# Kernel tuning notes

Hardware: AMD Instinct MI355X
Metric: run time of the kernel (lower is better)

Reference implementation:

```python
import jax, jax.numpy as jnp
import numpy as np

M, K, N = 32, 4096, 12288


def setup_inputs() -> dict:
    key = jax.random.key(0)
    k1, k2, k3, k4 = jax.random.split(key, 4)
    x = jax.random.normal(k1, (M, K), dtype=jnp.float32)
    # uint8-valued packed weight (stored as int32 for harness compatibility, values in [0,256))
    weight_u8 = jax.random.randint(k2, (K, N), 0, 256, dtype=jnp.int32)
    # per-output-channel fp16 scale and zero-point
    scale = (jax.random.uniform(k3, (N,), dtype=jnp.float32) * 0.01 + 1e-3).astype(jnp.float16)
    zero = (jax.random.uniform(k4, (N,), dtype=jnp.float32) * 255.0).astype(jnp.float16)
    return {"x": x, "weight_u8": weight_u8, "scale": scale, "zero": zero}


def reference(x, weight_u8, scale, zero):
    # QuantMatmulCustom: dequantize uint8 weight with per-channel fp16 scale/zero, then matmul.
    # w_deq[k, n] = (w_u8[k, n] - zero[n]) * scale[n]
    w_deq = (weight_u8.astype(jnp.float32) - zero.astype(jnp.float32)[None, :]) * scale.astype(jnp.float32)[None, :]
    # [M, K] @ [K, N] -> [M, N]
    return jnp.einsum('mk,kn->mn', x, w_deq)
```

## Files before the change

kernel.cpp:

```cpp
#include <hip/hip_runtime.h>

#define M_DIM 32
#define K_DIM 4096
#define N_DIM 12288
#define SPLITK 8
#define KPER  (K_DIM / SPLITK)
#define NT    (KPER / 32)
#define BLK   512
#define NPB   128

using bf16x8 = __attribute__((ext_vector_type(8))) short;
using f32x4  = __attribute__((ext_vector_type(4))) float;

__global__ __launch_bounds__(256) void qmm_zero(float* __restrict__ out) {
    int i = blockIdx.x * 256 + threadIdx.x;
    ((float4*)out)[i] = make_float4(0.f, 0.f, 0.f, 0.f);
}

__device__ __forceinline__ void load_b(const int* __restrict__ wp, int t, int (&wv)[8]) {
    #pragma unroll
    for (int j = 0; j < 8; ++j)
        wv[j] = wp[(size_t)(t * 32 + j) * N_DIM];
}

__device__ __forceinline__ bf16x8 pack_b(const int (&wv)[8]) {
    bf16x8 b;
    #pragma unroll
    for (int j = 0; j < 8; ++j) {
        float f = (float)wv[j];
        b[j] = (short)(__float_as_uint(f) >> 16);
    }
    return b;
}

__global__ __launch_bounds__(BLK, 6) void qmm_main(const float* __restrict__ x,
                                                   const int* __restrict__ w,
                                                   float* __restrict__ out) {
    __shared__ short lds_a[NT * 2 * 64 * 8];

    const int tid  = threadIdx.x;
    const int lane = tid & 63;
    const int g    = lane >> 4;
    const int c    = lane & 15;
    const int wid  = tid >> 6;
    const int k0   = blockIdx.y * KPER;
    const int n0   = blockIdx.x * NPB + wid * 16;

    for (int s = tid; s < NT * 2 * 64; s += BLK) {
        const int l  = s & 63;
        const int h  = (s >> 6) & 1;
        const int kt = s >> 7;
        const int m  = 16 * h + (l & 15);
        const float* xp = x + (size_t)m * K_DIM + k0 + kt * 32 + 8 * (l >> 4);
        bf16x8 v;
        #pragma unroll
        for (int j = 0; j < 8; ++j) {
            unsigned u = __float_as_uint(xp[j]);
            u += 0x7FFFu + ((u >> 16) & 1u);
            v[j] = (short)(u >> 16);
        }
        *(bf16x8*)&lds_a[s * 8] = v;
    }
    __syncthreads();

    f32x4 acc0 = {0.f, 0.f, 0.f, 0.f};
    f32x4 acc1 = {0.f, 0.f, 0.f, 0.f};

    const int*   wp = w + (size_t)(k0 + 8 * g) * N_DIM + n0 + c;
    const short* la = lds_a + lane * 8;

    int wvA[8], wvB[8];
    load_b(wp, 0, wvA);
    #pragma unroll
    for (int t = 0; t < NT; t += 2) {
        if (t + 1 < NT) load_b(wp, t + 1, wvB);
        {
            bf16x8 bf = pack_b(wvA);
            bf16x8 a0 = *(const bf16x8*)&la[(size_t)(t * 2 + 0) * 512];
            bf16x8 a1 = *(const bf16x8*)&la[(size_t)(t * 2 + 1) * 512];
            acc0 = __builtin_amdgcn_mfma_f32_16x16x32_bf16(a0, bf, acc0, 0, 0, 0);
            acc1 = __builtin_amdgcn_mfma_f32_16x16x32_bf16(a1, bf, acc1, 0, 0, 0);
        }
        if (t + 2 < NT) load_b(wp, t + 2, wvA);
        if (t + 1 < NT) {
            bf16x8 bf = pack_b(wvB);
            bf16x8 a0 = *(const bf16x8*)&la[(size_t)((t + 1) * 2 + 0) * 512];
            bf16x8 a1 = *(const bf16x8*)&la[(size_t)((t + 1) * 2 + 1) * 512];
            acc0 = __builtin_amdgcn_mfma_f32_16x16x32_bf16(a0, bf, acc0, 0, 0, 0);
            acc1 = __builtin_amdgcn_mfma_f32_16x16x32_bf16(a1, bf, acc1, 0, 0, 0);
        }
    }

    #pragma unroll
    for (int i = 0; i < 4; ++i) {
        const int r = 4 * (lane >> 4) + i;
        atomicAdd(&out[(size_t)r * N_DIM + n0 + c], acc0[i]);
        atomicAdd(&out[(size_t)(16 + r) * N_DIM + n0 + c], acc1[i]);
    }
}

__global__ __launch_bounds__(256) void qmm_scale(const float* __restrict__ x,
                                                 const float* __restrict__ scale,
                                                 const float* __restrict__ zero,
                                                 float* __restrict__ out) {
    const int m = blockIdx.y;
    __shared__ float red[256];
    float s = 0.f;
    for (int k = threadIdx.x; k < K_DIM; k += 256)
        s += x[(size_t)m * K_DIM + k];
    red[threadIdx.x] = s;
    __syncthreads();
    #pragma unroll
    for (int off = 128; off > 0; off >>= 1) {
        if (threadIdx.x < off) red[threadIdx.x] += red[threadIdx.x + off];
        __syncthreads();
    }
    const float rowsum = red[0];

    const int n = blockIdx.x * 256 + threadIdx.x;
    const float v = out[(size_t)m * N_DIM + n];
    out[(size_t)m * N_DIM + n] = scale[n] * (v - zero[n] * rowsum);
}

extern "C" void kernel_launch(void* const* d_in, const int* in_sizes, int n_in,
                              void* d_out, int out_size, void* d_ws, size_t ws_size,
                              hipStream_t stream) {
    const float* x     = (const float*)d_in[0];
    const int*   w     = (const int*)d_in[1];
    const float* scale = (const float*)d_in[2];
    const float* zero  = (const float*)d_in[3];
    float* out = (float*)d_out;

    qmm_zero <<<dim3((M_DIM * N_DIM / 4) / 256), dim3(256), 0, stream>>>(out);
    qmm_main <<<dim3(N_DIM / NPB, SPLITK),       dim3(BLK), 0, stream>>>(x, w, out);
    qmm_scale<<<dim3(N_DIM / 256, M_DIM),        dim3(256), 0, stream>>>(x, scale, zero, out);
}
```

Before: 53.21 us.

## Double split-K, deepen weight prefetch, and reduce partials via workspace

Split-K goes from 8 to 16, and launch bounds drop from 6 to 4 waves. The weight-load pipeline becomes a three-deep register ring, with the first loads issued before the LDS barrier so they overlap the activation staging. When the workspace is large enough, each split writes its partial tile to a workspace slice instead of atomically adding, and a finalize kernel sums the slices and applies the zero-point and scale corrections. This drops the zero-fill kernel and the atomics but adds 16×M×N of float partial traffic to write and read back, and the deeper prefetch needs more registers.

```diff
diff --git a/kernel.cpp b/kernel.cpp
--- a/kernel.cpp
+++ b/kernel.cpp
@@ -3,7 +3,7 @@
 #define M_DIM 32
 #define K_DIM 4096
 #define N_DIM 12288
-#define SPLITK 8
+#define SPLITK 16
 #define KPER  (K_DIM / SPLITK)
 #define NT    (KPER / 32)
 #define BLK   512
@@ -11,11 +11,6 @@
 
 using bf16x8 = __attribute__((ext_vector_type(8))) short;
 using f32x4  = __attribute__((ext_vector_type(4))) float;
-
-__global__ __launch_bounds__(256) void qmm_zero(float* __restrict__ out) {
-    int i = blockIdx.x * 256 + threadIdx.x;
-    ((float4*)out)[i] = make_float4(0.f, 0.f, 0.f, 0.f);
-}
 
 __device__ __forceinline__ void load_b(const int* __restrict__ wp, int t, int (&wv)[8]) {
     #pragma unroll
@@ -33,9 +28,10 @@
     return b;
 }
 
-__global__ __launch_bounds__(BLK, 6) void qmm_main(const float* __restrict__ x,
+template <bool WS>
+__global__ __launch_bounds__(BLK, 4) void qmm_main(const float* __restrict__ x,
                                                    const int* __restrict__ w,
-                                                   float* __restrict__ out) {
+                                                   float* __restrict__ dst) {
     __shared__ short lds_a[NT * 2 * 64 * 8];
 
     const int tid  = threadIdx.x;
@@ -61,44 +57,78 @@
         }
         *(bf16x8*)&lds_a[s * 8] = v;
     }
+
+    const int*   wp = w + (size_t)(k0 + 8 * g) * N_DIM + n0 + c;
+    const short* la = lds_a + lane * 8;
+
+    int wv[3][8];
+    load_b(wp, 0, wv[0]);
+    load_b(wp, 1, wv[1]);
+    load_b(wp, 2, wv[2]);
     __syncthreads();
 
     f32x4 acc0 = {0.f, 0.f, 0.f, 0.f};
     f32x4 acc1 = {0.f, 0.f, 0.f, 0.f};
 
-    const int*   wp = w + (size_t)(k0 + 8 * g) * N_DIM + n0 + c;
-    const short* la = lds_a + lane * 8;
-
-    int wvA[8], wvB[8];
-    load_b(wp, 0, wvA);
     #pragma unroll
-    for (int t = 0; t < NT; t += 2) {
-        if (t + 1 < NT) load_b(wp, t + 1, wvB);
-        {
-            bf16x8 bf = pack_b(wvA);
-            bf16x8 a0 = *(const bf16x8*)&la[(size_t)(t * 2 + 0) * 512];
-            bf16x8 a1 = *(const bf16x8*)&la[(size_t)(t * 2 + 1) * 512];
-            acc0 = __builtin_amdgcn_mfma_f32_16x16x32_bf16(a0, bf, acc0, 0, 0, 0);
-            acc1 = __builtin_amdgcn_mfma_f32_16x16x32_bf16(a1, bf, acc1, 0, 0, 0);
-        }
-        if (t + 2 < NT) load_b(wp, t + 2, wvA);
-        if (t + 1 < NT) {
-            bf16x8 bf = pack_b(wvB);
-            bf16x8 a0 = *(const bf16x8*)&la[(size_t)((t + 1) * 2 + 0) * 512];
-            bf16x8 a1 = *(const bf16x8*)&la[(size_t)((t + 1) * 2 + 1) * 512];
-            acc0 = __builtin_amdgcn_mfma_f32_16x16x32_bf16(a0, bf, acc0, 0, 0, 0);
-            acc1 = __builtin_amdgcn_mfma_f32_16x16x32_bf16(a1, bf, acc1, 0, 0, 0);
-        }
+    for (int t = 0; t < NT; ++t) {
+        bf16x8 bf = pack_b(wv[t % 3]);
+        if (t + 3 < NT) load_b(wp, t + 3, wv[t % 3]);
+        bf16x8 a0 = *(const bf16x8*)&la[(size_t)(t * 2 + 0) * 512];
+        bf16x8 a1 = *(const bf16x8*)&la[(size_t)(t * 2 + 1) * 512];
+        acc0 = __builtin_amdgcn_mfma_f32_16x16x32_bf16(a0, bf, acc0, 0, 0, 0);
+        acc1 = __builtin_amdgcn_mfma_f32_16x16x32_bf16(a1, bf, acc1, 0, 0, 0);
     }
 
-    #pragma unroll
-    for (int i = 0; i < 4; ++i) {
-        const int r = 4 * (lane >> 4) + i;
-        atomicAdd(&out[(size_t)r * N_DIM + n0 + c], acc0[i]);
-        atomicAdd(&out[(size_t)(16 + r) * N_DIM + n0 + c], acc1[i]);
+    if (WS) {
+        float* pp = dst + ((size_t)blockIdx.y * M_DIM) * N_DIM + n0 + c;
+        #pragma unroll
+        for (int i = 0; i < 4; ++i) {
+            const int r = 4 * (lane >> 4) + i;
+            pp[(size_t)r * N_DIM]        = acc0[i];
+            pp[(size_t)(16 + r) * N_DIM] = acc1[i];
+        }
+    } else {
+        #pragma unroll
+        for (int i = 0; i < 4; ++i) {
+            const int r = 4 * (lane >> 4) + i;
+            atomicAdd(&dst[(size_t)r * N_DIM + n0 + c], acc0[i]);
+            atomicAdd(&dst[(size_t)(16 + r) * N_DIM + n0 + c], acc1[i]);
+        }
     }
 }
 
+__global__ __launch_bounds__(256) void qmm_finalize(const float* __restrict__ part,
+                                                    const float* __restrict__ x,
+                                                    const float* __restrict__ scale,
+                                                    const float* __restrict__ zero,
+                                                    float* __restrict__ out) {
+    const int m = blockIdx.y;
+    __shared__ float red[256];
+    float s = 0.f;
+    for (int k = threadIdx.x; k < K_DIM; k += 256)
+        s += x[(size_t)m * K_DIM + k];
+    red[threadIdx.x] = s;
+    __syncthreads();
+    #pragma unroll
+    for (int off = 128; off > 0; off >>= 1) {
+        if (threadIdx.x < off) red[threadIdx.x] += red[threadIdx.x + off];
+        __syncthreads();
+    }
+    const float rowsum = red[0];
+
+    const int n = blockIdx.x * 256 + threadIdx.x;
+    float acc = 0.f;
+    #pragma unroll
+    for (int sp = 0; sp < SPLITK; ++sp)
+        acc += part[((size_t)sp * M_DIM + m) * N_DIM + n];
+    out[(size_t)m * N_DIM + n] = scale[n] * (acc - zero[n] * rowsum);
+}
+
+__global__ __launch_bounds__(256) void qmm_zero(float* __restrict__ out) {
+    int i = blockIdx.x * 256 + threadIdx.x;
+    ((float4*)out)[i] = make_float4(0.f, 0.f, 0.f, 0.f);
+}
 __global__ __launch_bounds__(256) void qmm_scale(const float* __restrict__ x,
                                                  const float* __restrict__ scale,
                                                  const float* __restrict__ zero,
@@ -116,7 +146,6 @@
         __syncthreads();
     }
     const float rowsum = red[0];
-
     const int n = blockIdx.x * 256 + threadIdx.x;
     const float v = out[(size_t)m * N_DIM + n];
     out[(size_t)m * N_DIM + n] = scale[n] * (v - zero[n] * rowsum);
@@ -131,7 +160,14 @@
     const float* zero  = (const float*)d_in[3];
     float* out = (float*)d_out;
 
-    qmm_zero <<<dim3((M_DIM * N_DIM / 4) / 256), dim3(256), 0, stream>>>(out);
-    qmm_main <<<dim3(N_DIM / NPB, SPLITK),       dim3(BLK), 0, stream>>>(x, w, out);
-    qmm_scale<<<dim3(N_DIM / 256, M_DIM),        dim3(256), 0, stream>>>(x, scale, zero, out);
+    const size_t need = (size_t)SPLITK * M_DIM * N_DIM * sizeof(float);
+    if (ws_size >= need) {
+        float* part = (float*)d_ws;
+        qmm_main<true><<<dim3(N_DIM / NPB, SPLITK), dim3(BLK), 0, stream>>>(x, w, part);
+        qmm_finalize<<<dim3(N_DIM / 256, M_DIM),    dim3(256), 0, stream>>>(part, x, scale, zero, out);
+    } else {
+        qmm_zero <<<dim3((M_DIM * N_DIM / 4) / 256),  dim3(256), 0, stream>>>(out);
+        qmm_main<false><<<dim3(N_DIM / NPB, SPLITK),  dim3(BLK), 0, stream>>>(x, w, out);
+        qmm_scale<<<dim3(N_DIM / 256, M_DIM),         dim3(256), 0, stream>>>(x, scale, zero, out);
+    }
 }
```

Result: faster. 48.59 us (-8.7%).
